# Optimization experiments

Measured on AMD Instinct MI355X. Metric: run time of the kernel, lower is better.

Reference implementation:

```python
import jax, jax.numpy as jnp
import numpy as np

B, S, DIM = 4, 2048, 64
NUM_CODES = 65536
KCODES = 8


def setup_inputs() -> dict:
    key = jax.random.key(0)
    k1, k2 = jax.random.split(key)
    x = jax.random.normal(k1, (B, S, DIM), dtype=jnp.float32)
    codebook = jax.random.normal(k2, (NUM_CODES, DIM), dtype=jnp.float32)
    return {"x": x, "codebook": codebook}


def reference(x, codebook):
    """EuclideanSnapFunction.forward, keep_k_codes path with no disabled codes.

    logits = -cdist(x, codebook, p=2); topk(kcodes); embedding gather; mean.
    sqrt is monotonic, so top-k on negative *squared* distance yields identical
    indices (and identical outputs) while avoiding the sqrt.
    """
    x2 = jnp.sum(x * x, axis=-1, keepdims=True)          # [B,S,1]
    c2 = jnp.sum(codebook * codebook, axis=-1)           # [N]
    xc = jnp.einsum("bsd,nd->bsn", x, codebook)          # [B,S,N]
    neg_d2 = 2.0 * xc - x2 - c2                           # = -squared dist
    _, codebook_ids = jax.lax.top_k(neg_d2, KCODES)      # [B,S,K]
    codes = codebook[codebook_ids]                        # [B,S,K,D] gather
    outputs = codes.sum(axis=-2) / KCODES                 # [B,S,D]
    return outputs, codebook_ids
```

## Files before the change

kernel.cpp:

```cpp
#include <hip/hip_runtime.h>
#include <float.h>

#define DIM     64
#define NCODES  65536
#define KC      8
#define NQ      8192
#define KROW    80
#define CS      64
#define CHUNK   (NCODES/CS)
#define NITER   (CHUNK/32)
#define NVIEW   128
#define CAP     7
#define DELTA   0.75f
#define MAXSUR  512
#define CSA     32
#define CHUNKA  512
#define NITERA  (CHUNKA/32)
#define NVIEWA  64

typedef __bf16 bf16x8 __attribute__((ext_vector_type(8)));
typedef float  f32x16 __attribute__((ext_vector_type(16)));
typedef unsigned short u16x8 __attribute__((ext_vector_type(8)));

#define ZERO16 {0,0,0,0, 0,0,0,0, 0,0,0,0, 0,0,0,0}

static __device__ __forceinline__ unsigned short f2bf(float f) {
    unsigned u = __float_as_uint(f);
    u += 0x7FFFu + ((u >> 16) & 1u);
    return (unsigned short)(u >> 16);
}

#define RJ(j) (((j) & 3) + 8 * ((j) >> 2))

__global__ __launch_bounds__(256) void k_conv_cb(const float* __restrict__ cb,
                                                 unsigned short* __restrict__ cbb) {
    int n = blockIdx.x * 256 + threadIdx.x;
    const float4* src = (const float4*)(cb + (size_t)n * DIM);
    unsigned short* dst = cbb + (size_t)n * KROW;
    float s = 0.f;
#pragma unroll
    for (int c = 0; c < 8; ++c) {
        float4 f0 = src[2 * c], f1 = src[2 * c + 1];
        s = fmaf(f0.x, f0.x, s); s = fmaf(f0.y, f0.y, s);
        s = fmaf(f0.z, f0.z, s); s = fmaf(f0.w, f0.w, s);
        s = fmaf(f1.x, f1.x, s); s = fmaf(f1.y, f1.y, s);
        s = fmaf(f1.z, f1.z, s); s = fmaf(f1.w, f1.w, s);
        u16x8 o;
        o[0] = f2bf(2.f * f0.x); o[1] = f2bf(2.f * f0.y);
        o[2] = f2bf(2.f * f0.z); o[3] = f2bf(2.f * f0.w);
        o[4] = f2bf(2.f * f1.x); o[5] = f2bf(2.f * f1.y);
        o[6] = f2bf(2.f * f1.z); o[7] = f2bf(2.f * f1.w);
        *(u16x8*)(dst + c * 8) = o;
    }
    unsigned short hi = f2bf(s);
    float hif = __uint_as_float(((unsigned)hi) << 16);
    unsigned short lo = f2bf(s - hif);
    u16x8 p = { (unsigned short)(hi ^ 0x8000u), (unsigned short)(lo ^ 0x8000u),
                0, 0, 0, 0, 0, 0 };
    *(u16x8*)(dst + 64) = p;
    u16x8 z = {0, 0, 0, 0, 0, 0, 0, 0};
    *(u16x8*)(dst + 72) = z;
}

__global__ __launch_bounds__(256) void k_conv_x(const float* __restrict__ x,
                                                unsigned short* __restrict__ xb) {
    int n = blockIdx.x * 256 + threadIdx.x;
    const float4* src = (const float4*)(x + (size_t)n * DIM);
    unsigned short* dst = xb + (size_t)n * KROW;
#pragma unroll
    for (int c = 0; c < 8; ++c) {
        float4 f0 = src[2 * c], f1 = src[2 * c + 1];
        u16x8 o;
        o[0] = f2bf(f0.x); o[1] = f2bf(f0.y); o[2] = f2bf(f0.z); o[3] = f2bf(f0.w);
        o[4] = f2bf(f1.x); o[5] = f2bf(f1.y); o[6] = f2bf(f1.z); o[7] = f2bf(f1.w);
        *(u16x8*)(dst + c * 8) = o;
    }
    u16x8 p = {0x3F80u, 0x3F80u, 0, 0, 0, 0, 0, 0};
    *(u16x8*)(dst + 64) = p;
    u16x8 z = {0, 0, 0, 0, 0, 0, 0, 0};
    *(u16x8*)(dst + 72) = z;
}

__device__ __forceinline__ float tmax16(const f32x16& a) {
    const float m0 = fmaxf(fmaxf(a[0],  a[1]),  a[2]);
    const float m1 = fmaxf(fmaxf(a[3],  a[4]),  a[5]);
    const float m2 = fmaxf(fmaxf(a[6],  a[7]),  a[8]);
    const float m3 = fmaxf(fmaxf(a[9],  a[10]), a[11]);
    const float m4 = fmaxf(fmaxf(a[12], a[13]), a[14]);
    const float n0 = fmaxf(fmaxf(m0, m1), m2);
    const float n1 = fmaxf(fmaxf(m3, m4), a[15]);
    return fmaxf(n0, n1);
}

#define LOAD10(t0, t1, tile) do {                                              \
    const __bf16* p0_ = abase + (size_t)(tile) * (32 * KROW);                  \
    const __bf16* p1_ = p0_ + 32 * KROW;                                       \
    _Pragma("unroll") for (int s_ = 0; s_ < 5; ++s_)                           \
        t0[s_] = *(const bf16x8*)(p0_ + s_ * 16);                              \
    _Pragma("unroll") for (int s_ = 0; s_ < 5; ++s_)                           \
        t1[s_] = *(const bf16x8*)(p1_ + s_ * 16);                              \
} while (0)

#define CLUSTER(c00, c01, c10, c11, t0, t1) do {                               \
    __builtin_amdgcn_s_setprio(1);                                             \
    _Pragma("unroll") for (int s_ = 0; s_ < 5; ++s_) {                         \
        c00 = __builtin_amdgcn_mfma_f32_32x32x16_bf16(t0[s_], bfrA[s_], c00, 0, 0, 0); \
        c01 = __builtin_amdgcn_mfma_f32_32x32x16_bf16(t0[s_], bfrB[s_], c01, 0, 0, 0); \
        c10 = __builtin_amdgcn_mfma_f32_32x32x16_bf16(t1[s_], bfrA[s_], c10, 0, 0, 0); \
        c11 = __builtin_amdgcn_mfma_f32_32x32x16_bf16(t1[s_], bfrB[s_], c11, 0, 0, 0); \
    }                                                                          \
    __builtin_amdgcn_s_setprio(0);                                             \
} while (0)

__global__ __launch_bounds__(256, 2) void k_scanA(const unsigned short* __restrict__ cbb_,
                                                  const unsigned short* __restrict__ xb_,
                                                  float* __restrict__ top1) {
    const __bf16* cbv = (const __bf16*)cbb_;
    const __bf16* xbv = (const __bf16*)xb_;
    const int tid = threadIdx.x, lane = tid & 63, wv = tid >> 6;
    const int laneh = lane >> 5, lrow = lane & 31;
    const int qg = blockIdx.x >> 5;
    const int cs = blockIdx.x & 31;
    const int qA = qg * 256 + wv * 64 + lrow;
    const int qB = qA + 32;
    const int cbase = cs * CHUNKA;
    const int view = cs * 2 + laneh;

    bf16x8 bfrA[5], bfrB[5];
    {
        const __bf16* bp = xbv + (size_t)qA * KROW + laneh * 8;
#pragma unroll
        for (int s = 0; s < 5; ++s) bfrA[s] = *(const bf16x8*)(bp + s * 16);
        bp += (size_t)32 * KROW;
#pragma unroll
        for (int s = 0; s < 5; ++s) bfrB[s] = *(const bf16x8*)(bp + s * 16);
    }

    float t1a = -FLT_MAX, t1b = -FLT_MAX;
    const __bf16* abase = cbv + (size_t)(cbase + lrow) * KROW + laneh * 8;

    bf16x8 fa0[5], fa1[5], fb0[5], fb1[5];
    LOAD10(fa0, fa1, 0);
    LOAD10(fb0, fb1, 2);

    for (int it = 0; it < NITERA; it += 4) {
        {
            f32x16 c00 = ZERO16, c01 = ZERO16, c10 = ZERO16, c11 = ZERO16;
            CLUSTER(c00, c01, c10, c11, fa0, fa1);
            LOAD10(fa0, fa1, it + 4);
            t1a = fmaxf(t1a, fmaxf(tmax16(c00), tmax16(c10)));
            t1b = fmaxf(t1b, fmaxf(tmax16(c01), tmax16(c11)));
        }
        {
            f32x16 c00 = ZERO16, c01 = ZERO16, c10 = ZERO16, c11 = ZERO16;
            CLUSTER(c00, c01, c10, c11, fb0, fb1);
            LOAD10(fb0, fb1, it + 6);
            t1a = fmaxf(t1a, fmaxf(tmax16(c00), tmax16(c10)));
            t1b = fmaxf(t1b, fmaxf(tmax16(c01), tmax16(c11)));
        }
    }

    top1[(size_t)qA * NVIEWA + view] = t1a;
    top1[(size_t)qB * NVIEWA + view] = t1b;
}

__global__ __launch_bounds__(256) void k_thresh(const float* __restrict__ top1,
                                                float* __restrict__ thrm) {
    const int lane = threadIdx.x & 63;
    const int q = blockIdx.x * 4 + (threadIdx.x >> 6);
    float v = top1[(size_t)q * NVIEWA + lane];
    float mx = -FLT_MAX;
#pragma unroll
    for (int r = 0; r < 8; ++r) {
        mx = v;
#pragma unroll
        for (int off = 32; off; off >>= 1) mx = fmaxf(mx, __shfl_xor(mx, off, 64));
        if (v == mx) v = -FLT_MAX;
    }
    if (lane == 0) thrm[q] = mx - DELTA;
}

__device__ __forceinline__ void coll_ep(const f32x16& acc, float Tm, int code0,
                                        unsigned short* __restrict__ buf, unsigned& c) {
    if (__any(tmax16(acc) >= Tm)) {
#pragma unroll
        for (int j = 0; j < 16; ++j)
            if (acc[j] >= Tm) { if (c < CAP) buf[c] = (unsigned short)(code0 + RJ(j)); ++c; }
    }
}

__global__ __launch_bounds__(256, 2) void k_collect(const unsigned short* __restrict__ cbb_,
                                                    const unsigned short* __restrict__ xb_,
                                                    const float* __restrict__ thrm,
                                                    unsigned short* __restrict__ cand,
                                                    unsigned char* __restrict__ cnt) {
    const __bf16* cbv = (const __bf16*)cbb_;
    const __bf16* xbv = (const __bf16*)xb_;
    const int tid = threadIdx.x, lane = tid & 63, wv = tid >> 6;
    const int laneh = lane >> 5, lrow = lane & 31;
    const int qg = blockIdx.x >> 6;
    const int cs = blockIdx.x & 63;
    const int qA = qg * 256 + wv * 64 + lrow;
    const int qB = qA + 32;
    const int cbase = cs * CHUNK;
    const int view = cs * 2 + laneh;

    bf16x8 bfrA[5], bfrB[5];
    {
        const __bf16* bp = xbv + (size_t)qA * KROW + laneh * 8;
#pragma unroll
        for (int s = 0; s < 5; ++s) bfrA[s] = *(const bf16x8*)(bp + s * 16);
        bp += (size_t)32 * KROW;
#pragma unroll
        for (int s = 0; s < 5; ++s) bfrB[s] = *(const bf16x8*)(bp + s * 16);
    }
    const float TmA = thrm[qA];
    const float TmB = thrm[qB];
    unsigned cA = 0, cB = 0;
    unsigned short* bufA = cand + ((size_t)qA * NVIEW + view) * CAP;
    unsigned short* bufB = cand + ((size_t)qB * NVIEW + view) * CAP;

    const __bf16* abase = cbv + (size_t)(cbase + lrow) * KROW + laneh * 8;

    bf16x8 fa0[5], fa1[5], fb0[5], fb1[5];
    LOAD10(fa0, fa1, 0);
    LOAD10(fb0, fb1, 2);

    for (int it = 0; it < NITER; it += 4) {
        {
            f32x16 c00 = ZERO16, c01 = ZERO16, c10 = ZERO16, c11 = ZERO16;
            CLUSTER(c00, c01, c10, c11, fa0, fa1);
            LOAD10(fa0, fa1, it + 4);
            const int code0 = cbase + it * 32 + 4 * laneh;
            coll_ep(c00, TmA, code0,      bufA, cA);
            coll_ep(c01, TmB, code0,      bufB, cB);
            coll_ep(c10, TmA, code0 + 32, bufA, cA);
            coll_ep(c11, TmB, code0 + 32, bufB, cB);
        }
        {
            f32x16 c00 = ZERO16, c01 = ZERO16, c10 = ZERO16, c11 = ZERO16;
            CLUSTER(c00, c01, c10, c11, fb0, fb1);
            LOAD10(fb0, fb1, it + 6);
            const int code0 = cbase + (it + 2) * 32 + 4 * laneh;
            coll_ep(c00, TmA, code0,      bufA, cA);
            coll_ep(c01, TmB, code0,      bufB, cB);
            coll_ep(c10, TmA, code0 + 32, bufA, cA);
            coll_ep(c11, TmB, code0 + 32, bufB, cB);
        }
    }
    cnt[(size_t)qA * NVIEW + view] = (unsigned char)(cA < CAP ? cA : CAP);
    cnt[(size_t)qB * NVIEW + view] = (unsigned char)(cB < CAP ? cB : CAP);
}

__device__ __forceinline__ float np_pairwise_sq64(const float* __restrict__ p) {
    float r[8];
#pragma unroll
    for (int j = 0; j < 8; ++j) r[j] = __fmul_rn(p[j], p[j]);
#pragma unroll
    for (int k = 1; k < 8; ++k)
#pragma unroll
        for (int j = 0; j < 8; ++j)
            r[j] = __fadd_rn(r[j], __fmul_rn(p[8 * k + j], p[8 * k + j]));
    const float t01 = __fadd_rn(r[0], r[1]);
    const float t23 = __fadd_rn(r[2], r[3]);
    const float t45 = __fadd_rn(r[4], r[5]);
    const float t67 = __fadd_rn(r[6], r[7]);
    return __fadd_rn(__fadd_rn(t01, t23), __fadd_rn(t45, t67));
}

__device__ __forceinline__ float score_key(const float* __restrict__ xr,
                                           const float* __restrict__ cr,
                                           float x2e) {
    float xc = 0.f;
#pragma unroll
    for (int d = 0; d < DIM; ++d) xc = __builtin_fmaf(cr[d], xr[d], xc);
    const float c2e = np_pairwise_sq64(cr);
    return __fsub_rn(__fsub_rn(__fmul_rn(2.0f, xc), x2e), c2e);
}

__global__ __launch_bounds__(256) void k_rescore(const float* __restrict__ x,
                                                 const float* __restrict__ cb,
                                                 const unsigned short* __restrict__ cand,
                                                 const unsigned char* __restrict__ cnt,
                                                 float* __restrict__ out0,
                                                 float* __restrict__ out1) {
    __shared__ int s_ids[4][MAXSUR];
    const int lane = threadIdx.x & 63;
    const int wvi = threadIdx.x >> 6;
    const int q = blockIdx.x * 4 + wvi;
    const float* xr = x + ((size_t)q << 6);
    const float x2e = np_pairwise_sq64(xr);

    const int c0 = cnt[(size_t)q * NVIEW + 2 * lane];
    const int c1 = cnt[(size_t)q * NVIEW + 2 * lane + 1];
    const int c = c0 + c1;
    int p = c;
#pragma unroll
    for (int off = 1; off < 64; off <<= 1) {
        const int t = __shfl_up(p, off, 64);
        if (lane >= off) p += t;
    }
    const int excl = p - c;
    int total = __shfl(p, 63, 64);
    if (total > MAXSUR) total = MAXSUR;
    const unsigned short* s0 = cand + ((size_t)q * NVIEW + 2 * lane) * CAP;
    for (int k = 0; k < c0; ++k) {
        const int dst = excl + k;
        if (dst < MAXSUR) s_ids[wvi][dst] = s0[k];
    }
    const unsigned short* s1 = s0 + CAP;
    for (int k = 0; k < c1; ++k) {
        const int dst = excl + c0 + k;
        if (dst < MAXSUR) s_ids[wvi][dst] = s1[k];
    }
    __syncthreads();

    float vv[8]; int id[8];
#pragma unroll
    for (int s = 0; s < 8; ++s) {
        vv[s] = -FLT_MAX; id[s] = 1 << 20;
        if (s * 64 < total) {
            const int pos = lane + 64 * s;
            if (pos < total) {
                const int idv = s_ids[wvi][pos];
                id[s] = idv;
                vv[s] = score_key(xr, cb + (size_t)idv * DIM, x2e);
            }
        }
    }

    double accd = 0.0;
#pragma unroll
    for (int rep = 0; rep < KC; ++rep) {
        float bv = vv[0]; int bi = id[0];
#pragma unroll
        for (int s = 1; s < 8; ++s)
            if (vv[s] > bv || (vv[s] == bv && id[s] < bi)) { bv = vv[s]; bi = id[s]; }
#pragma unroll
        for (int off = 32; off; off >>= 1) {
            const float ov = __shfl_xor(bv, off, 64);
            const int   oi = __shfl_xor(bi, off, 64);
            if (ov > bv || (ov == bv && oi < bi)) { bv = ov; bi = oi; }
        }
        if (lane == 0) out1[q * KC + rep] = (float)bi;
        accd += (double)cb[(size_t)bi * DIM + lane];
#pragma unroll
        for (int s = 0; s < 8; ++s) if (id[s] == bi) vv[s] = -FLT_MAX;
    }
    out0[(size_t)q * DIM + lane] = (float)(accd * 0.125);
}

extern "C" void kernel_launch(void* const* d_in, const int* in_sizes, int n_in,
                              void* d_out, int out_size, void* d_ws, size_t ws_size,
                              hipStream_t stream) {
    const float* x  = (const float*)d_in[0];
    const float* cb = (const float*)d_in[1];

    char* ws = (char*)d_ws;
    unsigned short* cbb  = (unsigned short*)ws;
    unsigned short* xb   = (unsigned short*)(ws + (size_t)NCODES * KROW * 2);
    float*          top1 = (float*)(ws + (size_t)NCODES * KROW * 2
                                       + (size_t)NQ * KROW * 2);
    float*          thrm = (float*)((char*)top1 + (size_t)NQ * NVIEWA * 4);
    unsigned char*  cnt  = (unsigned char*)((char*)thrm + (size_t)NQ * 4);
    unsigned short* cand = (unsigned short*)((char*)cnt + (size_t)NQ * NVIEW);

    float* out0 = (float*)d_out;
    float* out1 = (float*)d_out + (size_t)NQ * DIM;

    k_conv_cb<<<NCODES / 256, 256, 0, stream>>>(cb, cbb);
    k_conv_x <<<NQ / 256,     256, 0, stream>>>(x, xb);
    k_scanA  <<<1024,         256, 0, stream>>>(cbb, xb, top1);
    k_thresh <<<NQ / 4,       256, 0, stream>>>(top1, thrm);
    k_collect<<<2048,         256, 0, stream>>>(cbb, xb, thrm, cand, cnt);
    k_rescore<<<NQ / 4,       256, 0, stream>>>(x, cb, cand, cnt, out0, out1);
}
```

Measured before the change: 212.6 us.

## Shrink MFMA tiles to raise occupancy, triple-buffer loads, merge conversion kernels

The scan and collect kernels now compute one 32-code tile per stage with two accumulators instead of 2x2 tiles. Codebook fragment loads rotate through three register buffers, and launch bounds rise from 2 to 4 waves per SIMD, cutting register pressure so more waves can hide latency. The collect epilogue builds bitmasks and walks them with ctz instead of testing all 16 lanes one by one. The two conversion kernels are merged into one launch. The cost is less reuse of each loaded fragment per MFMA and possible spills under the tighter register budget.

```diff
diff --git a/kernel.cpp b/kernel.cpp
--- a/kernel.cpp
+++ b/kernel.cpp
@@ -32,53 +32,54 @@
 
 #define RJ(j) (((j) & 3) + 8 * ((j) >> 2))
 
-__global__ __launch_bounds__(256) void k_conv_cb(const float* __restrict__ cb,
-                                                 unsigned short* __restrict__ cbb) {
-    int n = blockIdx.x * 256 + threadIdx.x;
-    const float4* src = (const float4*)(cb + (size_t)n * DIM);
-    unsigned short* dst = cbb + (size_t)n * KROW;
-    float s = 0.f;
-#pragma unroll
-    for (int c = 0; c < 8; ++c) {
-        float4 f0 = src[2 * c], f1 = src[2 * c + 1];
-        s = fmaf(f0.x, f0.x, s); s = fmaf(f0.y, f0.y, s);
-        s = fmaf(f0.z, f0.z, s); s = fmaf(f0.w, f0.w, s);
-        s = fmaf(f1.x, f1.x, s); s = fmaf(f1.y, f1.y, s);
-        s = fmaf(f1.z, f1.z, s); s = fmaf(f1.w, f1.w, s);
-        u16x8 o;
-        o[0] = f2bf(2.f * f0.x); o[1] = f2bf(2.f * f0.y);
-        o[2] = f2bf(2.f * f0.z); o[3] = f2bf(2.f * f0.w);
-        o[4] = f2bf(2.f * f1.x); o[5] = f2bf(2.f * f1.y);
-        o[6] = f2bf(2.f * f1.z); o[7] = f2bf(2.f * f1.w);
-        *(u16x8*)(dst + c * 8) = o;
-    }
-    unsigned short hi = f2bf(s);
-    float hif = __uint_as_float(((unsigned)hi) << 16);
-    unsigned short lo = f2bf(s - hif);
-    u16x8 p = { (unsigned short)(hi ^ 0x8000u), (unsigned short)(lo ^ 0x8000u),
-                0, 0, 0, 0, 0, 0 };
-    *(u16x8*)(dst + 64) = p;
-    u16x8 z = {0, 0, 0, 0, 0, 0, 0, 0};
-    *(u16x8*)(dst + 72) = z;
-}
-
-__global__ __launch_bounds__(256) void k_conv_x(const float* __restrict__ x,
-                                                unsigned short* __restrict__ xb) {
-    int n = blockIdx.x * 256 + threadIdx.x;
-    const float4* src = (const float4*)(x + (size_t)n * DIM);
-    unsigned short* dst = xb + (size_t)n * KROW;
-#pragma unroll
-    for (int c = 0; c < 8; ++c) {
-        float4 f0 = src[2 * c], f1 = src[2 * c + 1];
-        u16x8 o;
-        o[0] = f2bf(f0.x); o[1] = f2bf(f0.y); o[2] = f2bf(f0.z); o[3] = f2bf(f0.w);
-        o[4] = f2bf(f1.x); o[5] = f2bf(f1.y); o[6] = f2bf(f1.z); o[7] = f2bf(f1.w);
-        *(u16x8*)(dst + c * 8) = o;
-    }
-    u16x8 p = {0x3F80u, 0x3F80u, 0, 0, 0, 0, 0, 0};
-    *(u16x8*)(dst + 64) = p;
-    u16x8 z = {0, 0, 0, 0, 0, 0, 0, 0};
-    *(u16x8*)(dst + 72) = z;
+__global__ __launch_bounds__(256) void k_conv(const float* __restrict__ cb,
+                                              const float* __restrict__ x,
+                                              unsigned short* __restrict__ cbb,
+                                              unsigned short* __restrict__ xb) {
+    if (blockIdx.x < NCODES / 256) {
+        int n = blockIdx.x * 256 + threadIdx.x;
+        const float4* src = (const float4*)(cb + (size_t)n * DIM);
+        unsigned short* dst = cbb + (size_t)n * KROW;
+        float s = 0.f;
+#pragma unroll
+        for (int c = 0; c < 8; ++c) {
+            float4 f0 = src[2 * c], f1 = src[2 * c + 1];
+            s = fmaf(f0.x, f0.x, s); s = fmaf(f0.y, f0.y, s);
+            s = fmaf(f0.z, f0.z, s); s = fmaf(f0.w, f0.w, s);
+            s = fmaf(f1.x, f1.x, s); s = fmaf(f1.y, f1.y, s);
+            s = fmaf(f1.z, f1.z, s); s = fmaf(f1.w, f1.w, s);
+            u16x8 o;
+            o[0] = f2bf(2.f * f0.x); o[1] = f2bf(2.f * f0.y);
+            o[2] = f2bf(2.f * f0.z); o[3] = f2bf(2.f * f0.w);
+            o[4] = f2bf(2.f * f1.x); o[5] = f2bf(2.f * f1.y);
+            o[6] = f2bf(2.f * f1.z); o[7] = f2bf(2.f * f1.w);
+            *(u16x8*)(dst + c * 8) = o;
+        }
+        unsigned short hi = f2bf(s);
+        float hif = __uint_as_float(((unsigned)hi) << 16);
+        unsigned short lo = f2bf(s - hif);
+        u16x8 p = { (unsigned short)(hi ^ 0x8000u), (unsigned short)(lo ^ 0x8000u),
+                    0, 0, 0, 0, 0, 0 };
+        *(u16x8*)(dst + 64) = p;
+        u16x8 z = {0, 0, 0, 0, 0, 0, 0, 0};
+        *(u16x8*)(dst + 72) = z;
+    } else {
+        int n = (blockIdx.x - NCODES / 256) * 256 + threadIdx.x;
+        const float4* src = (const float4*)(x + (size_t)n * DIM);
+        unsigned short* dst = xb + (size_t)n * KROW;
+#pragma unroll
+        for (int c = 0; c < 8; ++c) {
+            float4 f0 = src[2 * c], f1 = src[2 * c + 1];
+            u16x8 o;
+            o[0] = f2bf(f0.x); o[1] = f2bf(f0.y); o[2] = f2bf(f0.z); o[3] = f2bf(f0.w);
+            o[4] = f2bf(f1.x); o[5] = f2bf(f1.y); o[6] = f2bf(f1.z); o[7] = f2bf(f1.w);
+            *(u16x8*)(dst + c * 8) = o;
+        }
+        u16x8 p = {0x3F80u, 0x3F80u, 0, 0, 0, 0, 0, 0};
+        *(u16x8*)(dst + 64) = p;
+        u16x8 z = {0, 0, 0, 0, 0, 0, 0, 0};
+        *(u16x8*)(dst + 72) = z;
+    }
 }
 
 __device__ __forceinline__ float tmax16(const f32x16& a) {
@@ -92,27 +93,13 @@
     return fmaxf(n0, n1);
 }
 
-#define LOAD10(t0, t1, tile) do {                                              \
-    const __bf16* p0_ = abase + (size_t)(tile) * (32 * KROW);                  \
-    const __bf16* p1_ = p0_ + 32 * KROW;                                       \
+#define LOAD5(buf, tile) do {                                                  \
+    const __bf16* p_ = abase + (size_t)(tile) * (32 * KROW);                   \
     _Pragma("unroll") for (int s_ = 0; s_ < 5; ++s_)                           \
-        t0[s_] = *(const bf16x8*)(p0_ + s_ * 16);                              \
-    _Pragma("unroll") for (int s_ = 0; s_ < 5; ++s_)                           \
-        t1[s_] = *(const bf16x8*)(p1_ + s_ * 16);                              \
+        buf[s_] = *(const bf16x8*)(p_ + s_ * 16);                              \
 } while (0)
 
-#define CLUSTER(c00, c01, c10, c11, t0, t1) do {                               \
-    __builtin_amdgcn_s_setprio(1);                                             \
-    _Pragma("unroll") for (int s_ = 0; s_ < 5; ++s_) {                         \
-        c00 = __builtin_amdgcn_mfma_f32_32x32x16_bf16(t0[s_], bfrA[s_], c00, 0, 0, 0); \
-        c01 = __builtin_amdgcn_mfma_f32_32x32x16_bf16(t0[s_], bfrB[s_], c01, 0, 0, 0); \
-        c10 = __builtin_amdgcn_mfma_f32_32x32x16_bf16(t1[s_], bfrA[s_], c10, 0, 0, 0); \
-        c11 = __builtin_amdgcn_mfma_f32_32x32x16_bf16(t1[s_], bfrB[s_], c11, 0, 0, 0); \
-    }                                                                          \
-    __builtin_amdgcn_s_setprio(0);                                             \
-} while (0)
-
-__global__ __launch_bounds__(256, 2) void k_scanA(const unsigned short* __restrict__ cbb_,
+__global__ __launch_bounds__(256, 4) void k_scanA(const unsigned short* __restrict__ cbb_,
                                                   const unsigned short* __restrict__ xb_,
                                                   float* __restrict__ top1) {
     const __bf16* cbv = (const __bf16*)cbb_;
@@ -139,26 +126,26 @@
     float t1a = -FLT_MAX, t1b = -FLT_MAX;
     const __bf16* abase = cbv + (size_t)(cbase + lrow) * KROW + laneh * 8;
 
-    bf16x8 fa0[5], fa1[5], fb0[5], fb1[5];
-    LOAD10(fa0, fa1, 0);
-    LOAD10(fb0, fb1, 2);
-
-    for (int it = 0; it < NITERA; it += 4) {
-        {
-            f32x16 c00 = ZERO16, c01 = ZERO16, c10 = ZERO16, c11 = ZERO16;
-            CLUSTER(c00, c01, c10, c11, fa0, fa1);
-            LOAD10(fa0, fa1, it + 4);
-            t1a = fmaxf(t1a, fmaxf(tmax16(c00), tmax16(c10)));
-            t1b = fmaxf(t1b, fmaxf(tmax16(c01), tmax16(c11)));
-        }
-        {
-            f32x16 c00 = ZERO16, c01 = ZERO16, c10 = ZERO16, c11 = ZERO16;
-            CLUSTER(c00, c01, c10, c11, fb0, fb1);
-            LOAD10(fb0, fb1, it + 6);
-            t1a = fmaxf(t1a, fmaxf(tmax16(c00), tmax16(c10)));
-            t1b = fmaxf(t1b, fmaxf(tmax16(c01), tmax16(c11)));
-        }
-    }
+    bf16x8 fA[5], fB[5], fC[5];
+    LOAD5(fA, 0); LOAD5(fB, 1); LOAD5(fC, 2);
+
+#define SCANA_STAGE(buf, t) do {                                               \
+    f32x16 a0_ = ZERO16, a1_ = ZERO16;                                         \
+    _Pragma("unroll") for (int s_ = 0; s_ < 5; ++s_) {                         \
+        a0_ = __builtin_amdgcn_mfma_f32_32x32x16_bf16(buf[s_], bfrA[s_], a0_, 0, 0, 0); \
+        a1_ = __builtin_amdgcn_mfma_f32_32x32x16_bf16(buf[s_], bfrB[s_], a1_, 0, 0, 0); \
+    }                                                                          \
+    LOAD5(buf, (t) + 3);       \
+    t1a = fmaxf(t1a, tmax16(a0_));                                             \
+    t1b = fmaxf(t1b, tmax16(a1_));                                             \
+} while (0)
+
+    for (int t = 0; t < NITERA; t += 3) {
+        SCANA_STAGE(fA, t);
+        if (t + 1 < NITERA) SCANA_STAGE(fB, t + 1);
+        if (t + 2 < NITERA) SCANA_STAGE(fC, t + 2);
+    }
+#undef SCANA_STAGE
 
     top1[(size_t)qA * NVIEWA + view] = t1a;
     top1[(size_t)qB * NVIEWA + view] = t1b;
@@ -180,16 +167,7 @@
     if (lane == 0) thrm[q] = mx - DELTA;
 }
 
-__device__ __forceinline__ void coll_ep(const f32x16& acc, float Tm, int code0,
-                                        unsigned short* __restrict__ buf, unsigned& c) {
-    if (__any(tmax16(acc) >= Tm)) {
-#pragma unroll
-        for (int j = 0; j < 16; ++j)
-            if (acc[j] >= Tm) { if (c < CAP) buf[c] = (unsigned short)(code0 + RJ(j)); ++c; }
-    }
-}
-
-__global__ __launch_bounds__(256, 2) void k_collect(const unsigned short* __restrict__ cbb_,
+__global__ __launch_bounds__(256, 4) void k_collect(const unsigned short* __restrict__ cbb_,
                                                     const unsigned short* __restrict__ xb_,
                                                     const float* __restrict__ thrm,
                                                     unsigned short* __restrict__ cand,
@@ -222,32 +200,44 @@
 
     const __bf16* abase = cbv + (size_t)(cbase + lrow) * KROW + laneh * 8;
 
-    bf16x8 fa0[5], fa1[5], fb0[5], fb1[5];
-    LOAD10(fa0, fa1, 0);
-    LOAD10(fb0, fb1, 2);
-
-    for (int it = 0; it < NITER; it += 4) {
-        {
-            f32x16 c00 = ZERO16, c01 = ZERO16, c10 = ZERO16, c11 = ZERO16;
-            CLUSTER(c00, c01, c10, c11, fa0, fa1);
-            LOAD10(fa0, fa1, it + 4);
-            const int code0 = cbase + it * 32 + 4 * laneh;
-            coll_ep(c00, TmA, code0,      bufA, cA);
-            coll_ep(c01, TmB, code0,      bufB, cB);
-            coll_ep(c10, TmA, code0 + 32, bufA, cA);
-            coll_ep(c11, TmB, code0 + 32, bufB, cB);
-        }
-        {
-            f32x16 c00 = ZERO16, c01 = ZERO16, c10 = ZERO16, c11 = ZERO16;
-            CLUSTER(c00, c01, c10, c11, fb0, fb1);
-            LOAD10(fb0, fb1, it + 6);
-            const int code0 = cbase + (it + 2) * 32 + 4 * laneh;
-            coll_ep(c00, TmA, code0,      bufA, cA);
-            coll_ep(c01, TmB, code0,      bufB, cB);
-            coll_ep(c10, TmA, code0 + 32, bufA, cA);
-            coll_ep(c11, TmB, code0 + 32, bufB, cB);
-        }
-    }
+    bf16x8 fA[5], fB[5], fC[5];
+    LOAD5(fA, 0); LOAD5(fB, 1); LOAD5(fC, 2);
+
+#define COLL_STAGE(buf, t) do {                                                \
+    f32x16 a0_ = ZERO16, a1_ = ZERO16;                                         \
+    _Pragma("unroll") for (int s_ = 0; s_ < 5; ++s_) {                         \
+        a0_ = __builtin_amdgcn_mfma_f32_32x32x16_bf16(buf[s_], bfrA[s_], a0_, 0, 0, 0); \
+        a1_ = __builtin_amdgcn_mfma_f32_32x32x16_bf16(buf[s_], bfrB[s_], a1_, 0, 0, 0); \
+    }                                                                          \
+    LOAD5(buf, (t) + 3);       \
+    const float mA_ = tmax16(a0_), mB_ = tmax16(a1_);                          \
+    if (__any(fmaxf(mA_ - TmA, mB_ - TmB) >= 0.f)) {                           \
+        unsigned kA_ = 0, kB_ = 0;                                             \
+        _Pragma("unroll") for (int j_ = 0; j_ < 16; ++j_) {                    \
+            kA_ |= (a0_[j_] >= TmA) ? (1u << j_) : 0u;                         \
+            kB_ |= (a1_[j_] >= TmB) ? (1u << j_) : 0u;                         \
+        }                                                                      \
+        const int code0_ = cbase + (t) * 32 + 4 * laneh;                       \
+        while (kA_) {                                                          \
+            const int j_ = __builtin_ctz(kA_); kA_ &= kA_ - 1;                 \
+            if (cA < CAP) bufA[cA] = (unsigned short)(code0_ + RJ(j_));        \
+            ++cA;                                                              \
+        }                                                                      \
+        while (kB_) {                                                          \
+            const int j_ = __builtin_ctz(kB_); kB_ &= kB_ - 1;                 \
+            if (cB < CAP) bufB[cB] = (unsigned short)(code0_ + RJ(j_));        \
+            ++cB;                                                              \
+        }                                                                      \
+    }                                                                          \
+} while (0)
+
+    for (int t = 0; t < NITER; t += 3) {
+        COLL_STAGE(fA, t);
+        if (t + 1 < NITER) COLL_STAGE(fB, t + 1);
+        if (t + 2 < NITER) COLL_STAGE(fC, t + 2);
+    }
+#undef COLL_STAGE
+
     cnt[(size_t)qA * NVIEW + view] = (unsigned char)(cA < CAP ? cA : CAP);
     cnt[(size_t)qB * NVIEW + view] = (unsigned char)(cB < CAP ? cB : CAP);
 }
@@ -368,10 +358,9 @@
     float* out0 = (float*)d_out;
     float* out1 = (float*)d_out + (size_t)NQ * DIM;
 
-    k_conv_cb<<<NCODES / 256, 256, 0, stream>>>(cb, cbb);
-    k_conv_x <<<NQ / 256,     256, 0, stream>>>(x, xb);
-    k_scanA  <<<1024,         256, 0, stream>>>(cbb, xb, top1);
-    k_thresh <<<NQ / 4,       256, 0, stream>>>(top1, thrm);
-    k_collect<<<2048,         256, 0, stream>>>(cbb, xb, thrm, cand, cnt);
-    k_rescore<<<NQ / 4,       256, 0, stream>>>(x, cb, cand, cnt, out0, out1);
-}
+    k_conv   <<<NCODES / 256 + NQ / 256, 256, 0, stream>>>(cb, x, cbb, xb);
+    k_scanA  <<<1024,   256, 0, stream>>>(cbb, xb, top1);
+    k_thresh <<<NQ / 4, 256, 0, stream>>>(top1, thrm);
+    k_collect<<<2048,   256, 0, stream>>>(cbb, xb, thrm, cand, cnt);
+    k_rescore<<<NQ / 4, 256, 0, stream>>>(x, cb, cand, cnt, out0, out1);
+}
```

Result: slower. 394.4 us (+85.5%).
